# Performance work log

Hardware: AMD Instinct MI355X
Metric: run time of the kernel (lower is better)

## Reference

```python
import jax, jax.numpy as jnp
import numpy as np

N = 50000        # n_nodes
E = 800000       # n_edges (avg degree 16)
H = 64           # hidden_size
ALPHA = 0.5      # CRF alpha
BETA = 0.5       # CRF beta
N_LAYER = 2      # args.crf_layer
GAMMA = 0.2      # LeakyReLU negative slope


def setup_inputs() -> dict:
    key = jax.random.key(0)
    k = jax.random.split(key, 5)
    emb = jax.random.normal(k[0], (N, H), jnp.float32)
    W_fc = jax.random.normal(k[1], (H, H), jnp.float32) / np.sqrt(H)
    attn_fc_w = jax.random.normal(k[2], (1, 2 * H), jnp.float32) / np.sqrt(2 * H)
    src = jax.random.randint(k[3], (E,), 0, N, dtype=jnp.int32)
    dst = jax.random.randint(k[4], (E,), 0, N, dtype=jnp.int32)
    return {"emb": emb, "W_fc": W_fc, "attn_fc_w": attn_fc_w, "src": src, "dst": dst}


def _segment_softmax(e, dst, n):
    # softmax over incoming edges of each destination node (DGL mailbox softmax)
    m = jax.ops.segment_max(e, dst, num_segments=n)
    m = jnp.where(jnp.isfinite(m), m, 0.0)  # nodes with no in-edges
    ex = jnp.exp(e - m[dst])
    denom = jax.ops.segment_sum(ex, dst, num_segments=n)
    return ex / jnp.maximum(denom[dst], 1e-16)


def reference(emb, W_fc, attn_fc_w, src, dst):
    # attn_fc(concat(z_src, z_dst)) split into two per-node projections
    a_src = attn_fc_w[0, :H]
    a_dst = attn_fc_w[0, H:]
    h = emb
    e = None
    for _ in range(N_LAYER):
        z = h @ W_fc.T                              # [N, H] emb_attn
        e = (z @ a_src)[src] + (z @ a_dst)[dst]     # [E] edge logits
        e = jnp.where(e > 0, e, GAMMA * e)          # LeakyReLU(gamma)
        att = _segment_softmax(e, dst, N)           # [E]
        crf = jax.ops.segment_sum(att[:, None] * h[src], dst, num_segments=N)  # [N, H]
        h = (ALPHA * emb + BETA * crf) / (ALPHA + BETA)
    # training loss (is_train=True); reuses last layer's edge logits e
    loss_a = jnp.sum((h - emb) ** 2, axis=-1)                     # [N]
    att = _segment_softmax(e, dst, N)
    diff = jnp.sqrt(jnp.sum((h[dst] - h[src]) ** 2, axis=-1) + 1e-12)  # [E] L2 norm
    loss_b = jax.ops.segment_sum(att * diff, dst, num_segments=N)  # [N]
    loss = jnp.mean(ALPHA * loss_a + BETA * loss_b)
    return h, loss
```

## Files before the change

### kernel.cpp

```cpp
#include <hip/hip_runtime.h>

#define NNODES 50000
#define NEDGES 800000
#define HDIM 64
#define CAP 64
#define GAMMA 0.2f
#define SCAN_B 256
#define SCAN_NB ((NNODES + SCAN_B - 1) / SCAN_B)
#define LOSS_GRID 2048
#define NPART 8
#define NODES_PER_PART ((NNODES + NPART - 1) / NPART)
#define FILL_SLICES 192
#define E4 (NEDGES / 4)
#define CHUNK ((E4 + FILL_SLICES - 1) / FILL_SLICES)

typedef unsigned short u16;
typedef unsigned int u32;

__device__ __forceinline__ u16 f2bf(float f) {
    u32 u = __float_as_uint(f);
    u32 r = (u + 0x7FFFu + ((u >> 16) & 1u)) >> 16;
    return (u16)r;
}
__device__ __forceinline__ float bflo(u32 u) { return __uint_as_float(u << 16); }
__device__ __forceinline__ float bfhi(u32 u) { return __uint_as_float(u & 0xFFFF0000u); }

__device__ __forceinline__ float wave_sum(float v) {
    #pragma unroll
    for (int off = 32; off; off >>= 1) v += __shfl_xor(v, off, 64);
    return v;
}
__device__ __forceinline__ float wave_max(float v) {
    #pragma unroll
    for (int off = 32; off; off >>= 1) v = fmaxf(v, __shfl_xor(v, off, 64));
    return v;
}
__device__ __forceinline__ int wave_sum_i(int v) {
    #pragma unroll
    for (int off = 32; off; off >>= 1) v += __shfl_xor(v, off, 64);
    return v;
}
__device__ __forceinline__ float group8_sum(float v) {
    v += __shfl_xor(v, 1, 64);
    v += __shfl_xor(v, 2, 64);
    v += __shfl_xor(v, 4, 64);
    return v;
}

__global__ __launch_bounds__(256) void k_init(int* __restrict__ cursor,
                                              float* __restrict__ lossAcc,
                                              const float* __restrict__ Wfc,
                                              const float* __restrict__ attn,
                                              float* __restrict__ ws, float* __restrict__ wd) {
    int t = threadIdx.x;
    int idx = blockIdx.x * 256 + t;
    if (idx < NNODES) cursor[idx] = 0;
    if (blockIdx.x == gridDim.x - 1) {
        if (t >= 80 && t < 96) lossAcc[t - 80] = 0.f;
        if (t >= 128) {
            int tt = t - 128;
            int k = tt & 63;
            const float* av = attn + ((tt >= 64) ? HDIM : 0);
            float s = 0.f;
            for (int j = 0; j < HDIM; ++j) s += Wfc[j * HDIM + k] * av[j];
            if (tt < 64) ws[k] = s; else wd[k] = s;
        }
    }
}

__global__ __launch_bounds__(256) void k_fillx(const int4* __restrict__ src4,
                                               const int4* __restrict__ dst4,
                                               int* __restrict__ cursor,
                                               u16* __restrict__ padded,
                                               const float* __restrict__ emb,
                                               const float* __restrict__ ws,
                                               const float* __restrict__ wd,
                                               u16* __restrict__ emb_bf,
                                               float* __restrict__ zs, float* __restrict__ zd) {
    if (blockIdx.x < NPART * FILL_SLICES) {
        const int part = blockIdx.x & (NPART - 1);
        const int slice = blockIdx.x >> 3;
        const int lo = slice * CHUNK;
        const int hi = min(lo + CHUNK, E4);
        const int plo = part * NODES_PER_PART;
        const int phi = plo + NODES_PER_PART;
        for (int i = lo + threadIdx.x; i < hi; i += 256) {
            int4 s = src4[i];
            int4 d = dst4[i];
            if (d.x >= plo && d.x < phi) { int p0 = atomicAdd(&cursor[d.x], 1); if (p0 < CAP) padded[d.x * CAP + p0] = (u16)s.x; }
            if (d.y >= plo && d.y < phi) { int p1 = atomicAdd(&cursor[d.y], 1); if (p1 < CAP) padded[d.y * CAP + p1] = (u16)s.y; }
            if (d.z >= plo && d.z < phi) { int p2 = atomicAdd(&cursor[d.z], 1); if (p2 < CAP) padded[d.z * CAP + p2] = (u16)s.z; }
            if (d.w >= plo && d.w < phi) { int p3 = atomicAdd(&cursor[d.w], 1); if (p3 < CAP) padded[d.w * CAP + p3] = (u16)s.w; }
        }
    }
    int tid = blockIdx.x * blockDim.x + threadIdx.x;
    int wid = tid >> 6;
    int lane = tid & 63;
    if (wid < NNODES) {
        float v = emb[wid * HDIM + lane];
        emb_bf[wid * HDIM + lane] = f2bf(v);
        float a = wave_sum(v * ws[lane]);
        float b = wave_sum(v * wd[lane]);
        if (lane == 0) { zs[wid] = a; zd[wid] = b; }
    }
}

__global__ __launch_bounds__(SCAN_B) void k_scan1(const int* __restrict__ deg,
                                                  int* __restrict__ blockSums) {
    int t = threadIdx.x;
    int idx = blockIdx.x * SCAN_B + t;
    int v = (idx < NNODES) ? min(deg[idx], CAP) : 0;
    int ws = wave_sum_i(v);
    __shared__ int part[4];
    if ((t & 63) == 0) part[t >> 6] = ws;
    __syncthreads();
    if (t == 0) blockSums[blockIdx.x] = part[0] + part[1] + part[2] + part[3];
}

__global__ __launch_bounds__(SCAN_B) void k_scan2(int* __restrict__ blockSums,
                                                  int* __restrict__ blockOffs) {
    __shared__ int s[SCAN_B];
    int t = threadIdx.x;
    int v = (t < SCAN_NB) ? blockSums[t] : 0;
    s[t] = v;
    __syncthreads();
    for (int off = 1; off < SCAN_B; off <<= 1) {
        int x = (t >= off) ? s[t - off] : 0;
        __syncthreads();
        s[t] += x;
        __syncthreads();
    }
    if (t < SCAN_NB) blockOffs[t] = s[t] - v;
}

__global__ __launch_bounds__(SCAN_B) void k_scan3(const int* __restrict__ deg,
                                                  const int* __restrict__ blockOffs,
                                                  int* __restrict__ row_ptr) {
    __shared__ int s[SCAN_B];
    int t = threadIdx.x;
    int idx = blockIdx.x * SCAN_B + t;
    int v = (idx < NNODES) ? min(deg[idx], CAP) : 0;
    s[t] = v;
    __syncthreads();
    for (int off = 1; off < SCAN_B; off <<= 1) {
        int x = (t >= off) ? s[t - off] : 0;
        __syncthreads();
        s[t] += x;
        __syncthreads();
    }
    if (idx < NNODES) {
        int excl = s[t] - v + blockOffs[blockIdx.x];
        row_ptr[idx] = excl;
        if (idx == NNODES - 1) row_ptr[NNODES] = excl + v;
    }
}

template <bool STORE_ATT, bool COMPUTE_Z, bool WRITE_F32, bool STORE_LA, bool COMPACT>
__global__ __launch_bounds__(256) void k_layer(const u16* __restrict__ hbf_in,
                                               const float* __restrict__ emb,
                                               const int* __restrict__ deg,
                                               const int* __restrict__ row_ptr,
                                               const u16* __restrict__ padded,
                                               const float* __restrict__ zs,
                                               const float* __restrict__ zd,
                                               float* __restrict__ att_csr,
                                               u16* __restrict__ csr_c,
                                               u16* __restrict__ dmap_c,
                                               float* __restrict__ h_out,
                                               u16* __restrict__ hbf_out,
                                               const float* __restrict__ ws,
                                               const float* __restrict__ wd,
                                               float* __restrict__ zs_out,
                                               float* __restrict__ zd_out,
                                               float* __restrict__ la) {
    int wid = (blockIdx.x * blockDim.x + threadIdx.x) >> 6;
    int lane = threadIdx.x & 63;
    if (wid >= NNODES) return;
    int ne = min(deg[wid], CAP);
    int s0 = 0;
    if (STORE_ATT || COMPACT) s0 = row_ptr[wid];
    float zdn = zd[wid];
    const int sub8 = lane >> 3, q8 = lane & 7;
    float acc[8];
    #pragma unroll
    for (int i = 0; i < 8; ++i) acc[i] = 0.f;

    int s = 0; float e = -INFINITY;
    bool valid = lane < ne;
    if (valid) {
        s = padded[(size_t)wid * CAP + lane];
        float z = zs[s] + zdn;
        e = z > 0.f ? z : GAMMA * z;
    }
    float m = wave_max(e);
    float ex = valid ? __expf(e - m) : 0.f;
    float dsum = wave_sum(ex);
    float inv = 1.f / fmaxf(dsum, 1e-16f);
    if (STORE_ATT && valid) att_csr[s0 + lane] = ex * inv;
    if (COMPACT && valid) {
        csr_c[s0 + lane] = (u16)s;
        dmap_c[s0 + lane] = (u16)wid;
    }
    for (int j = 0; j < ne; j += 16) {
        int ja = j + sub8, jb = j + 8 + sub8;
        float wa = __shfl(ex, ja, 64);
        float wb = __shfl(ex, jb, 64);
        int ta = __shfl(s, ja, 64);
        int tb = __shfl(s, jb, 64);
        const uint4 ra = *(const uint4*)&hbf_in[(size_t)ta * HDIM + 8 * q8];
        const uint4 rb = *(const uint4*)&hbf_in[(size_t)tb * HDIM + 8 * q8];
        acc[0] += wa * bflo(ra.x) + wb * bflo(rb.x);
        acc[1] += wa * bfhi(ra.x) + wb * bfhi(rb.x);
        acc[2] += wa * bflo(ra.y) + wb * bflo(rb.y);
        acc[3] += wa * bfhi(ra.y) + wb * bfhi(rb.y);
        acc[4] += wa * bflo(ra.z) + wb * bflo(rb.z);
        acc[5] += wa * bfhi(ra.z) + wb * bfhi(rb.z);
        acc[6] += wa * bflo(ra.w) + wb * bflo(rb.w);
        acc[7] += wa * bfhi(ra.w) + wb * bfhi(rb.w);
    }
    #pragma unroll
    for (int off = 8; off <= 32; off <<= 1) {
        #pragma unroll
        for (int i = 0; i < 8; ++i) acc[i] += __shfl_xor(acc[i], off, 64);
    }
    float hv[8];
    #pragma unroll
    for (int i = 0; i < 8; ++i) hv[i] = 0.f;
    float lap = 0.f;
    if (sub8 == 0) {
        const float4 e0 = *(const float4*)&emb[(size_t)wid * HDIM + 8 * q8];
        const float4 e1 = *(const float4*)&emb[(size_t)wid * HDIM + 8 * q8 + 4];
        hv[0] = 0.5f * (e0.x + acc[0] * inv);
        hv[1] = 0.5f * (e0.y + acc[1] * inv);
        hv[2] = 0.5f * (e0.z + acc[2] * inv);
        hv[3] = 0.5f * (e0.w + acc[3] * inv);
        hv[4] = 0.5f * (e1.x + acc[4] * inv);
        hv[5] = 0.5f * (e1.y + acc[5] * inv);
        hv[6] = 0.5f * (e1.z + acc[6] * inv);
        hv[7] = 0.5f * (e1.w + acc[7] * inv);
        if (WRITE_F32) {
            *(float4*)&h_out[(size_t)wid * HDIM + 8 * q8]     = make_float4(hv[0], hv[1], hv[2], hv[3]);
            *(float4*)&h_out[(size_t)wid * HDIM + 8 * q8 + 4] = make_float4(hv[4], hv[5], hv[6], hv[7]);
        }
        uint4 o;
        o.x = (u32)f2bf(hv[0]) | ((u32)f2bf(hv[1]) << 16);
        o.y = (u32)f2bf(hv[2]) | ((u32)f2bf(hv[3]) << 16);
        o.z = (u32)f2bf(hv[4]) | ((u32)f2bf(hv[5]) << 16);
        o.w = (u32)f2bf(hv[6]) | ((u32)f2bf(hv[7]) << 16);
        *(uint4*)&hbf_out[(size_t)wid * HDIM + 8 * q8] = o;
        if (STORE_LA) {
            float d0 = hv[0] - e0.x, d1 = hv[1] - e0.y, d2 = hv[2] - e0.z, d3 = hv[3] - e0.w;
            float d4 = hv[4] - e1.x, d5 = hv[5] - e1.y, d6 = hv[6] - e1.z, d7 = hv[7] - e1.w;
            lap = d0 * d0 + d1 * d1 + d2 * d2 + d3 * d3 +
                  d4 * d4 + d5 * d5 + d6 * d6 + d7 * d7;
        }
    }
    if (STORE_LA) {
        float lsum = wave_sum(lap);
        if (lane == 0) la[wid] = lsum;
    }
    if (COMPUTE_Z) {
        float pa = 0.f, pb = 0.f;
        if (sub8 == 0) {
            const float4 w0 = *(const float4*)&ws[8 * q8];
            const float4 w1 = *(const float4*)&ws[8 * q8 + 4];
            const float4 d0 = *(const float4*)&wd[8 * q8];
            const float4 d1 = *(const float4*)&wd[8 * q8 + 4];
            pa = hv[0] * w0.x + hv[1] * w0.y + hv[2] * w0.z + hv[3] * w0.w +
                 hv[4] * w1.x + hv[5] * w1.y + hv[6] * w1.z + hv[7] * w1.w;
            pb = hv[0] * d0.x + hv[1] * d0.y + hv[2] * d0.z + hv[3] * d0.w +
                 hv[4] * d1.x + hv[5] * d1.y + hv[6] * d1.z + hv[7] * d1.w;
        }
        float a = wave_sum(pa);
        float b = wave_sum(pb);
        if (lane == 0) { zs_out[wid] = a; zd_out[wid] = b; }
    }
}

__global__ __launch_bounds__(256) void k_loss(const float* __restrict__ la,
                                              const u16* __restrict__ hbf,
                                              const u16* __restrict__ csr_src,
                                              const u16* __restrict__ dst_map,
                                              const float* __restrict__ att_csr,
                                              float* __restrict__ acc) {
    const int lane = threadIdx.x & 63;
    const int wib = threadIdx.x >> 6;
    const int gtid = blockIdx.x * blockDim.x + threadIdx.x;
    const int nthreads = gridDim.x * blockDim.x;
    const int gw = gtid >> 6;
    const int nwaves = nthreads >> 6;
    const int sub8 = lane >> 3, q8 = lane & 7;
    float lb = 0.f;

    for (int i = gtid; i < NNODES / 4; i += nthreads) {
        const float4 v = *(const float4*)&la[i * 4];
        lb += 0.5f * (v.x + v.y + v.z + v.w);
    }
    if ((NNODES & 3) != 0 && gtid < (NNODES & 3)) lb += 0.5f * la[(NNODES & ~3) + gtid];

    for (int g = gw; g < NEDGES / 32; g += nwaves) {
        int e0 = g * 32 + sub8;
        int e1 = e0 + 8, e2 = e0 + 16, e3 = e0 + 24;
        int s0i = csr_src[e0], d0i = dst_map[e0];
        int s1i = csr_src[e1], d1i = dst_map[e1];
        int s2i = csr_src[e2], d2i = dst_map[e2];
        int s3i = csr_src[e3], d3i = dst_map[e3];
        const uint4 rs0 = *(const uint4*)&hbf[(size_t)s0i * HDIM + 8 * q8];
        const uint4 rd0 = *(const uint4*)&hbf[(size_t)d0i * HDIM + 8 * q8];
        const uint4 rs1 = *(const uint4*)&hbf[(size_t)s1i * HDIM + 8 * q8];
        const uint4 rd1 = *(const uint4*)&hbf[(size_t)d1i * HDIM + 8 * q8];
        const uint4 rs2 = *(const uint4*)&hbf[(size_t)s2i * HDIM + 8 * q8];
        const uint4 rd2 = *(const uint4*)&hbf[(size_t)d2i * HDIM + 8 * q8];
        const uint4 rs3 = *(const uint4*)&hbf[(size_t)s3i * HDIM + 8 * q8];
        const uint4 rd3 = *(const uint4*)&hbf[(size_t)d3i * HDIM + 8 * q8];
        float a0 = bflo(rd0.x) - bflo(rs0.x), a1 = bfhi(rd0.x) - bfhi(rs0.x);
        float a2 = bflo(rd0.y) - bflo(rs0.y), a3 = bfhi(rd0.y) - bfhi(rs0.y);
        float a4 = bflo(rd0.z) - bflo(rs0.z), a5 = bfhi(rd0.z) - bfhi(rs0.z);
        float a6 = bflo(rd0.w) - bflo(rs0.w), a7 = bfhi(rd0.w) - bfhi(rs0.w);
        float b0 = bflo(rd1.x) - bflo(rs1.x), b1 = bfhi(rd1.x) - bfhi(rs1.x);
        float b2 = bflo(rd1.y) - bflo(rs1.y), b3 = bfhi(rd1.y) - bfhi(rs1.y);
        float b4 = bflo(rd1.z) - bflo(rs1.z), b5 = bfhi(rd1.z) - bfhi(rs1.z);
        float b6 = bflo(rd1.w) - bflo(rs1.w), b7 = bfhi(rd1.w) - bfhi(rs1.w);
        float c0 = bflo(rd2.x) - bflo(rs2.x), c1 = bfhi(rd2.x) - bfhi(rs2.x);
        float c2 = bflo(rd2.y) - bflo(rs2.y), c3 = bfhi(rd2.y) - bfhi(rs2.y);
        float c4 = bflo(rd2.z) - bflo(rs2.z), c5 = bfhi(rd2.z) - bfhi(rs2.z);
        float c6 = bflo(rd2.w) - bflo(rs2.w), c7 = bfhi(rd2.w) - bfhi(rs2.w);
        float g0 = bflo(rd3.x) - bflo(rs3.x), g1 = bfhi(rd3.x) - bfhi(rs3.x);
        float g2 = bflo(rd3.y) - bflo(rs3.y), g3 = bfhi(rd3.y) - bfhi(rs3.y);
        float g4 = bflo(rd3.z) - bflo(rs3.z), g5 = bfhi(rd3.z) - bfhi(rs3.z);
        float g6 = bflo(rd3.w) - bflo(rs3.w), g7 = bfhi(rd3.w) - bfhi(rs3.w);
        float ss0 = group8_sum(a0 * a0 + a1 * a1 + a2 * a2 + a3 * a3 +
                               a4 * a4 + a5 * a5 + a6 * a6 + a7 * a7);
        float ss1 = group8_sum(b0 * b0 + b1 * b1 + b2 * b2 + b3 * b3 +
                               b4 * b4 + b5 * b5 + b6 * b6 + b7 * b7);
        float ss2 = group8_sum(c0 * c0 + c1 * c1 + c2 * c2 + c3 * c3 +
                               c4 * c4 + c5 * c5 + c6 * c6 + c7 * c7);
        float ss3 = group8_sum(g0 * g0 + g1 * g1 + g2 * g2 + g3 * g3 +
                               g4 * g4 + g5 * g5 + g6 * g6 + g7 * g7);
        if (q8 == 0)
            lb += 0.5f * (att_csr[e0] * sqrtf(ss0 + 1e-12f) +
                          att_csr[e1] * sqrtf(ss1 + 1e-12f) +
                          att_csr[e2] * sqrtf(ss2 + 1e-12f) +
                          att_csr[e3] * sqrtf(ss3 + 1e-12f));
    }
    lb = wave_sum(lb);
    __shared__ float part[4];
    if (lane == 0) part[wib] = lb;
    __syncthreads();
    if (threadIdx.x == 0)
        atomicAdd(acc, part[0] + part[1] + part[2] + part[3]);
}

__global__ void k_finalize(const float* __restrict__ acc, float* __restrict__ out_loss) {
    out_loss[0] = acc[0] / (float)NNODES;
}

extern "C" void kernel_launch(void* const* d_in, const int* in_sizes, int n_in,
                              void* d_out, int out_size, void* d_ws, size_t ws_size,
                              hipStream_t stream) {
    const float* emb  = (const float*)d_in[0];
    const float* Wfc  = (const float*)d_in[1];
    const float* attn = (const float*)d_in[2];
    const int*   src  = (const int*)d_in[3];
    const int*   dst  = (const int*)d_in[4];
    float* out = (float*)d_out;

    char* p = (char*)d_ws;
    int*   cursor  = (int*)p;   p += (size_t)NNODES * 4;
    float* lossAcc = (float*)p; p += 256;
    int*   row_ptr = (int*)p;   p += (size_t)(NNODES + 1) * 4;
    int*   bsums   = (int*)p;   p += (size_t)SCAN_NB * 4;
    int*   boffs   = (int*)p;   p += (size_t)SCAN_NB * 4;
    float* wsv     = (float*)p; p += 64 * 4;
    float* wdv     = (float*)p; p += 64 * 4;
    float* zs0     = (float*)p; p += (size_t)NNODES * 4;
    float* zd0     = (float*)p; p += (size_t)NNODES * 4;
    float* zs1     = (float*)p; p += (size_t)NNODES * 4;
    float* zd1     = (float*)p; p += (size_t)NNODES * 4;
    float* laArr   = (float*)p; p += (size_t)NNODES * 4;
    float* att_csr = (float*)p; p += (size_t)NEDGES * 4;
    p = (char*)(((size_t)p + 255) & ~(size_t)255);
    u16*   padded  = (u16*)p;   p += (size_t)NNODES * CAP * 2;
    u16*   csr_src = (u16*)p;   p += (size_t)NEDGES * 2;
    u16*   dst_map = (u16*)p;   p += (size_t)NEDGES * 2;
    u16*   emb_bf  = (u16*)p;   p += (size_t)NNODES * HDIM * 2;
    u16*   h1_bf   = (u16*)p;   p += (size_t)NNODES * HDIM * 2;
    u16*   out_bf  = (u16*)p;   p += (size_t)NNODES * HDIM * 2;

    const int NB = (NNODES + 3) / 4;

    k_init<<<SCAN_NB, 256, 0, stream>>>(cursor, lossAcc, Wfc, attn, wsv, wdv);
    k_fillx<<<NB, 256, 0, stream>>>((const int4*)src, (const int4*)dst, cursor, padded,
                                    emb, wsv, wdv, emb_bf, zs0, zd0);
    k_scan1<<<SCAN_NB, SCAN_B, 0, stream>>>(cursor, bsums);
    k_scan2<<<1, SCAN_B, 0, stream>>>(bsums, boffs);
    k_scan3<<<SCAN_NB, SCAN_B, 0, stream>>>(cursor, boffs, row_ptr);

    k_layer<false, true, false, false, true><<<NB, 256, 0, stream>>>(
        emb_bf, emb, cursor, row_ptr, padded, zs0, zd0,
        att_csr, csr_src, dst_map, out , h1_bf, wsv, wdv, zs1, zd1, laArr);
    k_layer<true, false, true, true, false><<<NB, 256, 0, stream>>>(
        h1_bf, emb, cursor, row_ptr, padded, zs1, zd1,
        att_csr, csr_src, dst_map, out, out_bf, wsv, wdv, zs0, zd0, laArr);

    k_loss<<<LOSS_GRID, 256, 0, stream>>>(laArr, out_bf, csr_src, dst_map, att_csr, lossAcc);
    k_finalize<<<1, 1, 0, stream>>>(lossAcc, out + (size_t)NNODES * HDIM);
}
```

Measured before the change: 228.8 us.

## Regroup fill/scan kernels: move node projection into scan1, fold scan2 into scan3

```diff
diff --git a/kernel.cpp b/kernel.cpp
--- a/kernel.cpp
+++ b/kernel.cpp
@@ -71,27 +71,45 @@
 __global__ __launch_bounds__(256) void k_fillx(const int4* __restrict__ src4,
                                                const int4* __restrict__ dst4,
                                                int* __restrict__ cursor,
-                                               u16* __restrict__ padded,
-                                               const float* __restrict__ emb,
-                                               const float* __restrict__ ws,
-                                               const float* __restrict__ wd,
-                                               u16* __restrict__ emb_bf,
-                                               float* __restrict__ zs, float* __restrict__ zd) {
-    if (blockIdx.x < NPART * FILL_SLICES) {
-        const int part = blockIdx.x & (NPART - 1);
-        const int slice = blockIdx.x >> 3;
-        const int lo = slice * CHUNK;
-        const int hi = min(lo + CHUNK, E4);
-        const int plo = part * NODES_PER_PART;
-        const int phi = plo + NODES_PER_PART;
-        for (int i = lo + threadIdx.x; i < hi; i += 256) {
+                                               u16* __restrict__ padded) {
+    const int part = blockIdx.x & (NPART - 1);
+    const int slice = blockIdx.x >> 3;
+    const int lo = slice * CHUNK;
+    const int hi = min(lo + CHUNK, E4);
+    const int plo = part * NODES_PER_PART;
+    const int phi = plo + NODES_PER_PART;
+    for (int i = lo + threadIdx.x; i < hi; i += 256) {
+        int4 d = dst4[i];
+        bool mx = d.x >= plo && d.x < phi;
+        bool my = d.y >= plo && d.y < phi;
+        bool mz = d.z >= plo && d.z < phi;
+        bool mw = d.w >= plo && d.w < phi;
+        if (mx | my | mz | mw) {
             int4 s = src4[i];
-            int4 d = dst4[i];
-            if (d.x >= plo && d.x < phi) { int p0 = atomicAdd(&cursor[d.x], 1); if (p0 < CAP) padded[d.x * CAP + p0] = (u16)s.x; }
-            if (d.y >= plo && d.y < phi) { int p1 = atomicAdd(&cursor[d.y], 1); if (p1 < CAP) padded[d.y * CAP + p1] = (u16)s.y; }
-            if (d.z >= plo && d.z < phi) { int p2 = atomicAdd(&cursor[d.z], 1); if (p2 < CAP) padded[d.z * CAP + p2] = (u16)s.z; }
-            if (d.w >= plo && d.w < phi) { int p3 = atomicAdd(&cursor[d.w], 1); if (p3 < CAP) padded[d.w * CAP + p3] = (u16)s.w; }
+            if (mx) { int p0 = atomicAdd(&cursor[d.x], 1); if (p0 < CAP) padded[d.x * CAP + p0] = (u16)s.x; }
+            if (my) { int p1 = atomicAdd(&cursor[d.y], 1); if (p1 < CAP) padded[d.y * CAP + p1] = (u16)s.y; }
+            if (mz) { int p2 = atomicAdd(&cursor[d.z], 1); if (p2 < CAP) padded[d.z * CAP + p2] = (u16)s.z; }
+            if (mw) { int p3 = atomicAdd(&cursor[d.w], 1); if (p3 < CAP) padded[d.w * CAP + p3] = (u16)s.w; }
         }
+    }
+}
+
+__global__ __launch_bounds__(256) void k_scan1z(const int* __restrict__ deg,
+                                                int* __restrict__ blockSums,
+                                                const float* __restrict__ emb,
+                                                const float* __restrict__ ws,
+                                                const float* __restrict__ wd,
+                                                u16* __restrict__ emb_bf,
+                                                float* __restrict__ zs, float* __restrict__ zd) {
+    int t = threadIdx.x;
+    if (blockIdx.x < SCAN_NB) {
+        int idx = blockIdx.x * SCAN_B + t;
+        int v = (idx < NNODES) ? min(deg[idx], CAP) : 0;
+        int wsum = wave_sum_i(v);
+        __shared__ int part[4];
+        if ((t & 63) == 0) part[t >> 6] = wsum;
+        __syncthreads();
+        if (t == 0) blockSums[blockIdx.x] = part[0] + part[1] + part[2] + part[3];
     }
     int tid = blockIdx.x * blockDim.x + threadIdx.x;
     int wid = tid >> 6;
@@ -105,24 +123,13 @@
     }
 }
 
-__global__ __launch_bounds__(SCAN_B) void k_scan1(const int* __restrict__ deg,
-                                                  int* __restrict__ blockSums) {
-    int t = threadIdx.x;
-    int idx = blockIdx.x * SCAN_B + t;
-    int v = (idx < NNODES) ? min(deg[idx], CAP) : 0;
-    int ws = wave_sum_i(v);
-    __shared__ int part[4];
-    if ((t & 63) == 0) part[t >> 6] = ws;
-    __syncthreads();
-    if (t == 0) blockSums[blockIdx.x] = part[0] + part[1] + part[2] + part[3];
-}
-
-__global__ __launch_bounds__(SCAN_B) void k_scan2(int* __restrict__ blockSums,
-                                                  int* __restrict__ blockOffs) {
+__global__ __launch_bounds__(SCAN_B) void k_scan3(const int* __restrict__ deg,
+                                                  const int* __restrict__ blockSums,
+                                                  int* __restrict__ row_ptr) {
     __shared__ int s[SCAN_B];
     int t = threadIdx.x;
-    int v = (t < SCAN_NB) ? blockSums[t] : 0;
-    s[t] = v;
+    int bv = (t < SCAN_NB) ? blockSums[t] : 0;
+    s[t] = bv;
     __syncthreads();
     for (int off = 1; off < SCAN_B; off <<= 1) {
         int x = (t >= off) ? s[t - off] : 0;
@@ -130,14 +137,8 @@
         s[t] += x;
         __syncthreads();
     }
-    if (t < SCAN_NB) blockOffs[t] = s[t] - v;
-}
-
-__global__ __launch_bounds__(SCAN_B) void k_scan3(const int* __restrict__ deg,
-                                                  const int* __restrict__ blockOffs,
-                                                  int* __restrict__ row_ptr) {
-    __shared__ int s[SCAN_B];
-    int t = threadIdx.x;
+    int blockOff = (blockIdx.x > 0) ? s[blockIdx.x - 1] : 0;
+    __syncthreads();
     int idx = blockIdx.x * SCAN_B + t;
     int v = (idx < NNODES) ? min(deg[idx], CAP) : 0;
     s[t] = v;
@@ -149,7 +150,7 @@
         __syncthreads();
     }
     if (idx < NNODES) {
-        int excl = s[t] - v + blockOffs[blockIdx.x];
+        int excl = s[t] - v + blockOff;
         row_ptr[idx] = excl;
         if (idx == NNODES - 1) row_ptr[NNODES] = excl + v;
     }
@@ -370,7 +371,6 @@
     float* lossAcc = (float*)p; p += 256;
     int*   row_ptr = (int*)p;   p += (size_t)(NNODES + 1) * 4;
     int*   bsums   = (int*)p;   p += (size_t)SCAN_NB * 4;
-    int*   boffs   = (int*)p;   p += (size_t)SCAN_NB * 4;
     float* wsv     = (float*)p; p += 64 * 4;
     float* wdv     = (float*)p; p += 64 * 4;
     float* zs0     = (float*)p; p += (size_t)NNODES * 4;
@@ -390,11 +390,10 @@
     const int NB = (NNODES + 3) / 4;
 
     k_init<<<SCAN_NB, 256, 0, stream>>>(cursor, lossAcc, Wfc, attn, wsv, wdv);
-    k_fillx<<<NB, 256, 0, stream>>>((const int4*)src, (const int4*)dst, cursor, padded,
-                                    emb, wsv, wdv, emb_bf, zs0, zd0);
-    k_scan1<<<SCAN_NB, SCAN_B, 0, stream>>>(cursor, bsums);
-    k_scan2<<<1, SCAN_B, 0, stream>>>(bsums, boffs);
-    k_scan3<<<SCAN_NB, SCAN_B, 0, stream>>>(cursor, boffs, row_ptr);
+    k_fillx<<<NPART * FILL_SLICES, 256, 0, stream>>>((const int4*)src, (const int4*)dst,
+                                                     cursor, padded);
+    k_scan1z<<<NB, 256, 0, stream>>>(cursor, bsums, emb, wsv, wdv, emb_bf, zs0, zd0);
+    k_scan3<<<SCAN_NB, SCAN_B, 0, stream>>>(cursor, bsums, row_ptr);
 
     k_layer<false, true, false, false, true><<<NB, 256, 0, stream>>>(
         emb_bf, emb, cursor, row_ptr, padded, zs0, zd0,
```

Result: no change. 228.3 us, median of 2 (-0.2%).
